# Kernel optimization log

Hardware: AMD Instinct MI355X
Metric: run time of the kernel (lower is better)

The kernel has to match this reference:

```python
import jax, jax.numpy as jnp
import numpy as np

N = 2048          # target nodes
N_NODES = 2048    # neighbor pool
D_IN = 256
D_EDGE = 16
D_HID = 32
D_OUT = 256


def _mlp(h, w1, b1, w2, b2):
    # Linear -> Tanh -> Linear
    return jnp.tanh(h @ w1 + b1) @ w2 + b2


def setup_inputs() -> dict:
    key = jax.random.key(0)
    ks = jax.random.split(key, 20)
    s = 0.05
    inp = {
        "x": jax.random.normal(ks[0], (N, D_IN), jnp.float32),
        "neibs": jax.random.normal(ks[1], (N_NODES, D_IN), jnp.float32),
        "edge_emb": jax.random.normal(ks[2], (N * N_NODES, D_EDGE), jnp.float32),
        # multiplicative binary mask (float, as in original ws * mask)
        "mask": (jax.random.uniform(ks[3], (N, N_NODES)) < 0.7).astype(jnp.float32),
        "ax_w1": jax.random.normal(ks[4], (D_IN, D_HID), jnp.float32) * s,
        "ax_b1": jnp.zeros((D_HID,), jnp.float32),
        "ax_w2": jax.random.normal(ks[5], (D_HID, D_HID), jnp.float32) * s,
        "ax_b2": jnp.zeros((D_HID,), jnp.float32),
        "an_w1": jax.random.normal(ks[6], (D_IN, D_HID), jnp.float32) * s,
        "an_b1": jnp.zeros((D_HID,), jnp.float32),
        "an_w2": jax.random.normal(ks[7], (D_HID, D_HID), jnp.float32) * s,
        "an_b2": jnp.zeros((D_HID,), jnp.float32),
        "ae_w1": jax.random.normal(ks[8], (D_EDGE, D_HID), jnp.float32) * s,
        "ae_b1": jnp.zeros((D_HID,), jnp.float32),
        "ae_w2": jax.random.normal(ks[9], (D_HID, D_HID), jnp.float32) * s,
        "ae_b2": jnp.zeros((D_HID,), jnp.float32),
        "fcx_w": jax.random.normal(ks[10], (2 * D_IN, D_OUT), jnp.float32) * s,
        "fcx_b": jnp.zeros((D_OUT,), jnp.float32),
    }
    return inp


def reference(x, neibs, edge_emb, mask,
              ax_w1, ax_b1, ax_w2, ax_b2,
              an_w1, an_b1, an_w2, an_b2,
              ae_w1, ae_b1, ae_w2, ae_b2,
              fcx_w, fcx_b):
    x_att = _mlp(x, ax_w1, ax_b1, ax_w2, ax_b2)          # (N, H)
    neib_att = _mlp(neibs, an_w1, an_b1, an_w2, an_b2)   # (n_nodes, H)
    # edge attention is computed in the original forward but never used (dead code)
    _edge_att = _mlp(edge_emb, ae_w1, ae_b1, ae_w2, ae_b2)
    # multiplicative masking (NOT additive -inf), then softmax over neighbors
    ws = jnp.einsum('nh,mh->nm', x_att, neib_att) * mask  # (N, n_nodes)
    ws = jax.nn.softmax(ws, axis=1)
    agg_neib = jax.nn.sigmoid(ws @ neibs)                 # (N, D_IN)
    # concat_node=False path: concat -> fc_x -> sigmoid; dropout is identity (eval)
    out = jax.nn.sigmoid(jnp.concatenate([x, agg_neib], axis=1) @ fcx_w + fcx_b)
    return out
```

## Files before the change

kernel.cpp:

```cpp
#include <hip/hip_runtime.h>
#include <hip/hip_bf16.h>
#include <math.h>

#define NROWS 2048
#define DIN 256
#define DH 32
#define DOUT 256

typedef unsigned short ushort_t;
typedef unsigned int uint_t;
typedef __attribute__((ext_vector_type(8))) short short8;
typedef __attribute__((ext_vector_type(4))) float floatx4;

__device__ __forceinline__ float bf2f(uint_t u) {
    union { uint_t i; float f; } v; v.i = u << 16; return v.f;
}
__device__ __forceinline__ ushort_t f2bf(float f) {
    __hip_bfloat16 h = __float2bfloat16(f);
    union { __hip_bfloat16 h; ushort_t u; } v; v.h = h; return v.u;
}
__device__ __forceinline__ float sigm(float v) { return 1.0f / (1.0f + __expf(-v)); }

#define PSTR 2056
#define ASTR 520

__global__ __launch_bounds__(256) void prep_kernel(
    const float* __restrict__ x, const float* __restrict__ neibs,
    const float* __restrict__ ax_w1, const float* __restrict__ ax_b1,
    const float* __restrict__ ax_w2, const float* __restrict__ ax_b2,
    const float* __restrict__ an_w1, const float* __restrict__ an_b1,
    const float* __restrict__ an_w2, const float* __restrict__ an_b2,
    const float* __restrict__ fcx_w,
    ushort_t* __restrict__ x_attB, short8* __restrict__ n_attP,
    short8* __restrict__ B_pack, short8* __restrict__ W_pack)
{
    __shared__ float smem[32 * 256];
    const int t = threadIdx.x;
    const int b = blockIdx.x;

    if (b < 512) {
        float (*srow)[DIN] = (float (*)[DIN])smem;
        float* hbuf = smem + 8 * DIN;
        float* sbuf = smem + 8 * DIN + 8 * DH;

        const bool is_x = b < 256;
        const int row0 = (is_x ? b : b - 256) * 8;
        const float* __restrict__ in = is_x ? x : neibs;
        const float* __restrict__ w1 = is_x ? ax_w1 : an_w1;
        const float* __restrict__ b1 = is_x ? ax_b1 : an_b1;
        const float* __restrict__ w2 = is_x ? ax_w2 : an_w2;
        const float* __restrict__ b2 = is_x ? ax_b2 : an_b2;

        const int r = t >> 5, c = t & 31;
        {
            const float4* in4 = (const float4*)(in + (size_t)(row0 + r) * DIN);
            float4 a = in4[c * 2], bb = in4[c * 2 + 1];
            *(float4*)&srow[r][c * 8] = a;
            *(float4*)&srow[r][c * 8 + 4] = bb;
        }
        __syncthreads();

        float s = b1[c];
#pragma unroll 8
        for (int k = 0; k < DIN; ++k) s += srow[r][k] * w1[k * DH + c];
        s = tanhf(s);
        hbuf[r * DH + c] = s;
        __syncthreads();

        float s2 = b2[c];
#pragma unroll
        for (int j = 0; j < DH; ++j) s2 += hbuf[r * DH + j] * w2[j * DH + c];

        if (is_x) {
            x_attB[(size_t)(row0 + r) * DH + c] = f2bf(s2);
        } else {
            sbuf[r * DH + c] = s2;
            __syncthreads();
            if (t < 32) {
                const int r2 = t >> 2, q = t & 3;
                const int row = row0 + r2;
                short8 v;
#pragma unroll
                for (int j = 0; j < 8; ++j) v[j] = (short)f2bf(sbuf[r2 * DH + q * 8 + j]);
                n_attP[(row >> 4) * 64 + q * 16 + (row & 15)] = v;
            }
        }
    } else if (b < 576) {
        const int s = b - 512;
        float* tile = smem;
#pragma unroll
        for (int i = 0; i < 8; ++i) {
            const int e = i * 256 + t;
            const int row = e >> 6, c4 = e & 63;
            const float4 v = ((const float4*)neibs)[(size_t)(32 * s + row) * 64 + c4];
            *(float4*)&tile[row * 256 + c4 * 4] = v;
        }
        __syncthreads();
#pragma unroll
        for (int i = 0; i < 4; ++i) {
            const int G = i * 256 + t;
            const int n = G & 15, q = (G >> 4) & 3, tt = (G >> 6) & 3, w = G >> 8;
            const int col = w * 64 + tt * 16 + n;
            short8 v;
#pragma unroll
            for (int j = 0; j < 8; ++j) v[j] = (short)f2bf(tile[(8 * q + j) * 256 + col]);
            B_pack[s * 1024 + G] = v;
        }
    } else {
        const int s = b - 576;
        float* tile = smem;
#pragma unroll
        for (int i = 0; i < 8; ++i) {
            const int e = i * 256 + t;
            const int row = e >> 6, c4 = e & 63;
            const float4 v = ((const float4*)fcx_w)[(size_t)(32 * s + row) * 64 + c4];
            *(float4*)&tile[row * 256 + c4 * 4] = v;
        }
        __syncthreads();
#pragma unroll
        for (int i = 0; i < 4; ++i) {
            const int G = i * 256 + t;
            const int n = G & 15, q = (G >> 4) & 3, tt = (G >> 6) & 3, w = G >> 8;
            const int col = w * 64 + tt * 16 + n;
            short8 v;
#pragma unroll
            for (int j = 0; j < 8; ++j) v[j] = (short)f2bf(tile[(8 * q + j) * 256 + col]);
            W_pack[s * 1024 + G] = v;
        }
    }
}

__global__ __launch_bounds__(512, 2) void attn_kernel(
    const float* __restrict__ x, const float* __restrict__ mask,
    const ushort_t* __restrict__ x_attB, const short8* __restrict__ n_attP,
    const short8* __restrict__ B_pack, const short8* __restrict__ W_pack,
    const float* __restrict__ fcx_b, float* __restrict__ out)
{
    __shared__ __align__(16) ushort_t pTr[8 * PSTR];
    __shared__ __align__(16) ushort_t ATr[8 * ASTR];
    __shared__ float row_inv[8];

    const int t = threadIdx.x;
    const int n0 = blockIdx.x * 8;
    const int w = t >> 6, lane = t & 63;
    const int q = lane >> 4, nn = lane & 15;
    const int arow = lane & 7;
    const int rbase = (lane >> 4) * 4;

#pragma unroll
    for (int i = 0; i < 4; ++i) {
        const int e = i * 512 + t;
        const int r = e >> 8, k = e & 255;
        ATr[r * ASTR + k] = f2bf(x[(size_t)(n0 + r) * DIN + k]);
    }

    const short8 av_s = *(const short8*)(x_attB + (size_t)(n0 + arow) * DH + q * 8);
#pragma unroll 4
    for (int i = 0; i < 16; ++i) {
        const int tl = w * 16 + i;
        const short8 bv = n_attP[tl * 64 + lane];
        floatx4 c = __builtin_amdgcn_mfma_f32_16x16x32_bf16(
            av_s, bv, (floatx4){0.f, 0.f, 0.f, 0.f}, 0, 0, 0);
        if (lane < 32) {
            const int m = tl * 16 + nn;
#pragma unroll
            for (int rg = 0; rg < 4; ++rg) {
                const int row = rbase + rg;
                const float sv = c[rg] * mask[(size_t)(n0 + row) * NROWS + m];
                pTr[row * PSTR + m] = f2bf(sv);
            }
        }
    }
    __syncthreads();

    {
        ushort_t* prow = pTr + w * PSTR;
        uint_t raw[16];
        float mx = -1e30f;
#pragma unroll
        for (int j = 0; j < 16; ++j) {
            raw[j] = *(const uint_t*)(prow + j * 128 + 2 * lane);
            mx = fmaxf(mx, fmaxf(bf2f(raw[j] & 0xffffu), bf2f(raw[j] >> 16)));
        }
#pragma unroll
        for (int off = 32; off >= 1; off >>= 1) mx = fmaxf(mx, __shfl_xor(mx, off));
        float sum = 0.f;
#pragma unroll
        for (int j = 0; j < 16; ++j) {
            const float e0 = __expf(bf2f(raw[j] & 0xffffu) - mx);
            const float e1 = __expf(bf2f(raw[j] >> 16) - mx);
            sum += e0 + e1;
            *(uint_t*)(prow + j * 128 + 2 * lane) =
                (uint_t)f2bf(e0) | ((uint_t)f2bf(e1) << 16);
        }
#pragma unroll
        for (int off = 32; off >= 1; off >>= 1) sum += __shfl_xor(sum, off);
        if (lane == 0) row_inv[w] = 1.f / sum;
    }
    __syncthreads();

    const int cq = w & 3, kh = w >> 2;
    const char* aBase = (const char*)pTr + arow * (PSTR * 2);
    floatx4 acc[4];
#pragma unroll
    for (int tt = 0; tt < 4; ++tt) acc[tt] = (floatx4){0.f, 0.f, 0.f, 0.f};

#pragma unroll 4
    for (int si = 0; si < 32; ++si) {
        const int s = kh * 32 + si;
        const short8 av = *(const short8*)(aBase + s * 64 + q * 16);
#pragma unroll
        for (int tt = 0; tt < 4; ++tt) {
            const short8 bv = B_pack[(s * 16 + cq * 4 + tt) * 64 + lane];
            acc[tt] = __builtin_amdgcn_mfma_f32_16x16x32_bf16(av, bv, acc[tt], 0, 0, 0);
        }
    }
    __syncthreads();
    float* red = (float*)pTr;
    if (kh == 1) {
#pragma unroll
        for (int tt = 0; tt < 4; ++tt)
            *(floatx4*)&red[((cq * 4 + tt) * 64 + lane) * 4] = acc[tt];
    }
    __syncthreads();
    if (kh == 0) {
#pragma unroll
        for (int tt = 0; tt < 4; ++tt) {
            const floatx4 rv = *(const floatx4*)&red[((cq * 4 + tt) * 64 + lane) * 4];
            acc[tt] += rv;
        }
        if (lane < 32) {
#pragma unroll
            for (int tt = 0; tt < 4; ++tt) {
                const int n = cq * 64 + tt * 16 + nn;
#pragma unroll
                for (int rg = 0; rg < 4; ++rg) {
                    const int row = rbase + rg;
                    ATr[row * ASTR + 256 + n] = f2bf(sigm(acc[tt][rg] * row_inv[row]));
                }
            }
        }
    }
    __syncthreads();

    const char* a2 = (const char*)ATr + arow * (ASTR * 2);
    floatx4 acc2[4];
#pragma unroll
    for (int tt = 0; tt < 4; ++tt) acc2[tt] = (floatx4){0.f, 0.f, 0.f, 0.f};

#pragma unroll
    for (int si = 0; si < 8; ++si) {
        const int s = kh * 8 + si;
        const short8 av = *(const short8*)(a2 + s * 64 + q * 16);
#pragma unroll
        for (int tt = 0; tt < 4; ++tt) {
            const short8 bv = W_pack[(s * 16 + cq * 4 + tt) * 64 + lane];
            acc2[tt] = __builtin_amdgcn_mfma_f32_16x16x32_bf16(av, bv, acc2[tt], 0, 0, 0);
        }
    }
    __syncthreads();
    if (kh == 1) {
#pragma unroll
        for (int tt = 0; tt < 4; ++tt)
            *(floatx4*)&red[((cq * 4 + tt) * 64 + lane) * 4] = acc2[tt];
    }
    __syncthreads();
    if (kh == 0) {
#pragma unroll
        for (int tt = 0; tt < 4; ++tt) {
            const floatx4 rv = *(const floatx4*)&red[((cq * 4 + tt) * 64 + lane) * 4];
            acc2[tt] += rv;
        }
        if (lane < 32) {
#pragma unroll
            for (int tt = 0; tt < 4; ++tt) {
                const int n = cq * 64 + tt * 16 + nn;
                const float bias = fcx_b[n];
#pragma unroll
                for (int rg = 0; rg < 4; ++rg) {
                    const int row = rbase + rg;
                    out[(size_t)(n0 + row) * DOUT + n] = sigm(acc2[tt][rg] + bias);
                }
            }
        }
    }
}

extern "C" void kernel_launch(void* const* d_in, const int* in_sizes, int n_in,
                              void* d_out, int out_size, void* d_ws, size_t ws_size,
                              hipStream_t stream) {
    const float* x      = (const float*)d_in[0];
    const float* neibs  = (const float*)d_in[1];
    const float* mask   = (const float*)d_in[3];
    const float* ax_w1  = (const float*)d_in[4];
    const float* ax_b1  = (const float*)d_in[5];
    const float* ax_w2  = (const float*)d_in[6];
    const float* ax_b2  = (const float*)d_in[7];
    const float* an_w1  = (const float*)d_in[8];
    const float* an_b1  = (const float*)d_in[9];
    const float* an_w2  = (const float*)d_in[10];
    const float* an_b2  = (const float*)d_in[11];
    const float* fcx_w  = (const float*)d_in[16];
    const float* fcx_b  = (const float*)d_in[17];
    float* out = (float*)d_out;

    char* ws = (char*)d_ws;
    ushort_t* x_attB = (ushort_t*)ws;
    short8*   n_attP = (short8*)(ws + 131072);
    short8*   B_pack = (short8*)(ws + 262144);
    short8*   W_pack = (short8*)(ws + 1310720);

    prep_kernel<<<592, 256, 0, stream>>>(
        x, neibs, ax_w1, ax_b1, ax_w2, ax_b2,
        an_w1, an_b1, an_w2, an_b2, fcx_w,
        x_attB, n_attP, B_pack, W_pack);

    attn_kernel<<<256, 512, 0, stream>>>(
        x, mask, x_attB, n_attP, B_pack, W_pack, fcx_b, out);
}
```

Baseline: 384.1 us.

## Split fused attention kernel into score, PV and FC GEMM kernels

Replaces the single fused attention kernel with three kernels. The first computes masked scores and the softmax, then writes normalized probabilities to a packed global buffer. The second does the P·neibs GEMM on 32-row by 64-column tiles, and the third does the final FC GEMM; x is converted to bf16 into a shared concat buffer during prep. The aim is to stop each 8-row block from streaming the whole packed neighbor matrix, which cuts L2/HBM traffic for B and raises MFMA reuse. In exchange it adds two kernel launches and a global round-trip for the probability and concat intermediates.

```diff
diff --git a/kernel.cpp b/kernel.cpp
--- a/kernel.cpp
+++ b/kernel.cpp
@@ -21,8 +21,7 @@
 }
 __device__ __forceinline__ float sigm(float v) { return 1.0f / (1.0f + __expf(-v)); }
 
-#define PSTR 2056
-#define ASTR 520
+#define PST 2056
 
 __global__ __launch_bounds__(256) void prep_kernel(
     const float* __restrict__ x, const float* __restrict__ neibs,
@@ -32,7 +31,8 @@
     const float* __restrict__ an_w2, const float* __restrict__ an_b2,
     const float* __restrict__ fcx_w,
     ushort_t* __restrict__ x_attB, short8* __restrict__ n_attP,
-    short8* __restrict__ B_pack, short8* __restrict__ W_pack)
+    short8* __restrict__ B_pack, short8* __restrict__ W_pack,
+    ushort_t* __restrict__ XA)
 {
     __shared__ float smem[32 * 256];
     const int t = threadIdx.x;
@@ -99,14 +99,14 @@
 #pragma unroll
         for (int i = 0; i < 4; ++i) {
             const int G = i * 256 + t;
-            const int n = G & 15, q = (G >> 4) & 3, tt = (G >> 6) & 3, w = G >> 8;
-            const int col = w * 64 + tt * 16 + n;
+            const int n = G & 15, q = (G >> 4) & 3, tl = G >> 6;
+            const int col = tl * 16 + n;
             short8 v;
 #pragma unroll
             for (int j = 0; j < 8; ++j) v[j] = (short)f2bf(tile[(8 * q + j) * 256 + col]);
-            B_pack[s * 1024 + G] = v;
-        }
-    } else {
+            B_pack[(size_t)(s * 16 + tl) * 64 + q * 16 + n] = v;
+        }
+    } else if (b < 592) {
         const int s = b - 576;
         float* tile = smem;
 #pragma unroll
@@ -120,169 +120,176 @@
 #pragma unroll
         for (int i = 0; i < 4; ++i) {
             const int G = i * 256 + t;
-            const int n = G & 15, q = (G >> 4) & 3, tt = (G >> 6) & 3, w = G >> 8;
-            const int col = w * 64 + tt * 16 + n;
+            const int n = G & 15, q = (G >> 4) & 3, tl = G >> 6;
+            const int col = tl * 16 + n;
             short8 v;
 #pragma unroll
             for (int j = 0; j < 8; ++j) v[j] = (short)f2bf(tile[(8 * q + j) * 256 + col]);
-            W_pack[s * 1024 + G] = v;
-        }
-    }
-}
-
-__global__ __launch_bounds__(512, 2) void attn_kernel(
-    const float* __restrict__ x, const float* __restrict__ mask,
+            W_pack[(size_t)(s * 16 + tl) * 64 + q * 16 + n] = v;
+        }
+    } else {
+        const int base = (b - 592) * 32;
+#pragma unroll
+        for (int j = 0; j < 32; ++j) {
+            const int row = base + j;
+            XA[(size_t)row * 512 + t] = f2bf(x[(size_t)row * DIN + t]);
+        }
+    }
+}
+
+__global__ __launch_bounds__(256) void score_kernel(
+    const float* __restrict__ mask,
     const ushort_t* __restrict__ x_attB, const short8* __restrict__ n_attP,
-    const short8* __restrict__ B_pack, const short8* __restrict__ W_pack,
+    short8* __restrict__ P_pack)
+{
+    __shared__ __align__(16) ushort_t pT[8 * PST];
+    __shared__ float row_inv[8];
+
+    const int t = threadIdx.x, b = blockIdx.x;
+    const int n0 = b * 8;
+    const int w = t >> 6, lane = t & 63;
+    const int q = lane >> 4, nn = lane & 15;
+
+    const short8 av = *(const short8*)(x_attB + (size_t)(n0 + (lane & 7)) * DH + q * 8);
+
+#pragma unroll 4
+    for (int i = 0; i < 32; ++i) {
+        const int tl = w * 32 + i;
+        const short8 bv = n_attP[tl * 64 + lane];
+        floatx4 c = __builtin_amdgcn_mfma_f32_16x16x32_bf16(
+            av, bv, (floatx4){0.f, 0.f, 0.f, 0.f}, 0, 0, 0);
+        if (lane < 32) {
+            const int m = tl * 16 + nn;
+            const int rbase = (lane >> 4) * 4;
+#pragma unroll
+            for (int rg = 0; rg < 4; ++rg) {
+                const int r = rbase + rg;
+                const float sv = c[rg] * mask[(size_t)(n0 + r) * NROWS + m];
+                pT[r * PST + m] = f2bf(sv);
+            }
+        }
+    }
+    __syncthreads();
+
+    {
+        const int r0 = 2 * w, r1 = r0 + 1;
+        ushort_t* p0 = pT + r0 * PST;
+        ushort_t* p1 = pT + r1 * PST;
+        float mx0 = -1e30f, mx1 = -1e30f;
+        uint_t raw0[16], raw1[16];
+#pragma unroll
+        for (int j = 0; j < 16; ++j) {
+            raw0[j] = *(const uint_t*)(p0 + j * 128 + 2 * lane);
+            raw1[j] = *(const uint_t*)(p1 + j * 128 + 2 * lane);
+            mx0 = fmaxf(mx0, fmaxf(bf2f(raw0[j] & 0xffffu), bf2f(raw0[j] >> 16)));
+            mx1 = fmaxf(mx1, fmaxf(bf2f(raw1[j] & 0xffffu), bf2f(raw1[j] >> 16)));
+        }
+#pragma unroll
+        for (int off = 32; off >= 1; off >>= 1) {
+            mx0 = fmaxf(mx0, __shfl_xor(mx0, off));
+            mx1 = fmaxf(mx1, __shfl_xor(mx1, off));
+        }
+        float l0 = 0.f, l1 = 0.f;
+#pragma unroll
+        for (int j = 0; j < 16; ++j) {
+            const float e00 = __expf(bf2f(raw0[j] & 0xffffu) - mx0);
+            const float e01 = __expf(bf2f(raw0[j] >> 16) - mx0);
+            const float e10 = __expf(bf2f(raw1[j] & 0xffffu) - mx1);
+            const float e11 = __expf(bf2f(raw1[j] >> 16) - mx1);
+            l0 += e00 + e01; l1 += e10 + e11;
+            *(uint_t*)(p0 + j * 128 + 2 * lane) = (uint_t)f2bf(e00) | ((uint_t)f2bf(e01) << 16);
+            *(uint_t*)(p1 + j * 128 + 2 * lane) = (uint_t)f2bf(e10) | ((uint_t)f2bf(e11) << 16);
+        }
+#pragma unroll
+        for (int off = 32; off >= 1; off >>= 1) {
+            l0 += __shfl_xor(l0, off);
+            l1 += __shfl_xor(l1, off);
+        }
+        if (lane == 0) { row_inv[r0] = 1.f / l0; row_inv[r1] = 1.f / l1; }
+    }
+    __syncthreads();
+
+    const int rt16 = b >> 1, h = b & 1;
+    const int sr = nn;
+    if ((sr >> 3) == h) {
+        const float invr = row_inv[sr & 7];
+        const ushort_t* prow = pT + (sr & 7) * PST;
+#pragma unroll
+        for (int i = 0; i < 16; ++i) {
+            const int s = w * 16 + i;
+            const short8 e = *(const short8*)(prow + 32 * s + 8 * q);
+            short8 v;
+#pragma unroll
+            for (int j = 0; j < 8; ++j)
+                v[j] = (short)f2bf(bf2f((uint_t)(ushort_t)e[j]) * invr);
+            P_pack[(size_t)(rt16 * 64 + s) * 64 + lane] = v;
+        }
+    }
+}
+
+__global__ __launch_bounds__(256) void pv_kernel(
+    const short8* __restrict__ P_pack, const short8* __restrict__ B_pack,
+    ushort_t* __restrict__ XA)
+{
+    const int t = threadIdx.x, b = blockIdx.x;
+    const int rt32 = b >> 2, cs = b & 3;
+    const int w = t >> 6, lane = t & 63;
+    const int ct = cs * 4 + w;
+
+    const short8* PA0 = P_pack + (size_t)(2 * rt32) * 64 * 64;
+    const short8* PA1 = PA0 + 64 * 64;
+
+    floatx4 a0 = (floatx4){0.f, 0.f, 0.f, 0.f};
+    floatx4 a1 = (floatx4){0.f, 0.f, 0.f, 0.f};
+#pragma unroll 4
+    for (int s = 0; s < 64; ++s) {
+        const short8 A0 = PA0[s * 64 + lane];
+        const short8 A1 = PA1[s * 64 + lane];
+        const short8 B  = B_pack[(size_t)(s * 16 + ct) * 64 + lane];
+        a0 = __builtin_amdgcn_mfma_f32_16x16x32_bf16(A0, B, a0, 0, 0, 0);
+        a1 = __builtin_amdgcn_mfma_f32_16x16x32_bf16(A1, B, a1, 0, 0, 0);
+    }
+
+    const int col = 16 * ct + (lane & 15);
+    const int rb = (lane >> 4) * 4;
+#pragma unroll
+    for (int rg = 0; rg < 4; ++rg) {
+        XA[(size_t)(32 * rt32 + rb + rg) * 512 + 256 + col] = f2bf(sigm(a0[rg]));
+        XA[(size_t)(32 * rt32 + 16 + rb + rg) * 512 + 256 + col] = f2bf(sigm(a1[rg]));
+    }
+}
+
+__global__ __launch_bounds__(256) void fc_kernel(
+    const ushort_t* __restrict__ XA, const short8* __restrict__ W_pack,
     const float* __restrict__ fcx_b, float* __restrict__ out)
 {
-    __shared__ __align__(16) ushort_t pTr[8 * PSTR];
-    __shared__ __align__(16) ushort_t ATr[8 * ASTR];
-    __shared__ float row_inv[8];
-
-    const int t = threadIdx.x;
-    const int n0 = blockIdx.x * 8;
+    const int t = threadIdx.x, b = blockIdx.x;
+    const int rt32 = b >> 2, cs = b & 3;
     const int w = t >> 6, lane = t & 63;
+    const int ct = cs * 4 + w;
     const int q = lane >> 4, nn = lane & 15;
-    const int arow = lane & 7;
-    const int rbase = (lane >> 4) * 4;
-
-#pragma unroll
-    for (int i = 0; i < 4; ++i) {
-        const int e = i * 512 + t;
-        const int r = e >> 8, k = e & 255;
-        ATr[r * ASTR + k] = f2bf(x[(size_t)(n0 + r) * DIN + k]);
-    }
-
-    const short8 av_s = *(const short8*)(x_attB + (size_t)(n0 + arow) * DH + q * 8);
-#pragma unroll 4
-    for (int i = 0; i < 16; ++i) {
-        const int tl = w * 16 + i;
-        const short8 bv = n_attP[tl * 64 + lane];
-        floatx4 c = __builtin_amdgcn_mfma_f32_16x16x32_bf16(
-            av_s, bv, (floatx4){0.f, 0.f, 0.f, 0.f}, 0, 0, 0);
-        if (lane < 32) {
-            const int m = tl * 16 + nn;
-#pragma unroll
-            for (int rg = 0; rg < 4; ++rg) {
-                const int row = rbase + rg;
-                const float sv = c[rg] * mask[(size_t)(n0 + row) * NROWS + m];
-                pTr[row * PSTR + m] = f2bf(sv);
-            }
-        }
-    }
-    __syncthreads();
-
-    {
-        ushort_t* prow = pTr + w * PSTR;
-        uint_t raw[16];
-        float mx = -1e30f;
-#pragma unroll
-        for (int j = 0; j < 16; ++j) {
-            raw[j] = *(const uint_t*)(prow + j * 128 + 2 * lane);
-            mx = fmaxf(mx, fmaxf(bf2f(raw[j] & 0xffffu), bf2f(raw[j] >> 16)));
-        }
-#pragma unroll
-        for (int off = 32; off >= 1; off >>= 1) mx = fmaxf(mx, __shfl_xor(mx, off));
-        float sum = 0.f;
-#pragma unroll
-        for (int j = 0; j < 16; ++j) {
-            const float e0 = __expf(bf2f(raw[j] & 0xffffu) - mx);
-            const float e1 = __expf(bf2f(raw[j] >> 16) - mx);
-            sum += e0 + e1;
-            *(uint_t*)(prow + j * 128 + 2 * lane) =
-                (uint_t)f2bf(e0) | ((uint_t)f2bf(e1) << 16);
-        }
-#pragma unroll
-        for (int off = 32; off >= 1; off >>= 1) sum += __shfl_xor(sum, off);
-        if (lane == 0) row_inv[w] = 1.f / sum;
-    }
-    __syncthreads();
-
-    const int cq = w & 3, kh = w >> 2;
-    const char* aBase = (const char*)pTr + arow * (PSTR * 2);
-    floatx4 acc[4];
-#pragma unroll
-    for (int tt = 0; tt < 4; ++tt) acc[tt] = (floatx4){0.f, 0.f, 0.f, 0.f};
-
-#pragma unroll 4
-    for (int si = 0; si < 32; ++si) {
-        const int s = kh * 32 + si;
-        const short8 av = *(const short8*)(aBase + s * 64 + q * 16);
-#pragma unroll
-        for (int tt = 0; tt < 4; ++tt) {
-            const short8 bv = B_pack[(s * 16 + cq * 4 + tt) * 64 + lane];
-            acc[tt] = __builtin_amdgcn_mfma_f32_16x16x32_bf16(av, bv, acc[tt], 0, 0, 0);
-        }
-    }
-    __syncthreads();
-    float* red = (float*)pTr;
-    if (kh == 1) {
-#pragma unroll
-        for (int tt = 0; tt < 4; ++tt)
-            *(floatx4*)&red[((cq * 4 + tt) * 64 + lane) * 4] = acc[tt];
-    }
-    __syncthreads();
-    if (kh == 0) {
-#pragma unroll
-        for (int tt = 0; tt < 4; ++tt) {
-            const floatx4 rv = *(const floatx4*)&red[((cq * 4 + tt) * 64 + lane) * 4];
-            acc[tt] += rv;
-        }
-        if (lane < 32) {
-#pragma unroll
-            for (int tt = 0; tt < 4; ++tt) {
-                const int n = cq * 64 + tt * 16 + nn;
-#pragma unroll
-                for (int rg = 0; rg < 4; ++rg) {
-                    const int row = rbase + rg;
-                    ATr[row * ASTR + 256 + n] = f2bf(sigm(acc[tt][rg] * row_inv[row]));
-                }
-            }
-        }
-    }
-    __syncthreads();
-
-    const char* a2 = (const char*)ATr + arow * (ASTR * 2);
-    floatx4 acc2[4];
-#pragma unroll
-    for (int tt = 0; tt < 4; ++tt) acc2[tt] = (floatx4){0.f, 0.f, 0.f, 0.f};
-
-#pragma unroll
-    for (int si = 0; si < 8; ++si) {
-        const int s = kh * 8 + si;
-        const short8 av = *(const short8*)(a2 + s * 64 + q * 16);
-#pragma unroll
-        for (int tt = 0; tt < 4; ++tt) {
-            const short8 bv = W_pack[(s * 16 + cq * 4 + tt) * 64 + lane];
-            acc2[tt] = __builtin_amdgcn_mfma_f32_16x16x32_bf16(av, bv, acc2[tt], 0, 0, 0);
-        }
-    }
-    __syncthreads();
-    if (kh == 1) {
-#pragma unroll
-        for (int tt = 0; tt < 4; ++tt)
-            *(floatx4*)&red[((cq * 4 + tt) * 64 + lane) * 4] = acc2[tt];
-    }
-    __syncthreads();
-    if (kh == 0) {
-#pragma unroll
-        for (int tt = 0; tt < 4; ++tt) {
-            const floatx4 rv = *(const floatx4*)&red[((cq * 4 + tt) * 64 + lane) * 4];
-            acc2[tt] += rv;
-        }
-        if (lane < 32) {
-#pragma unroll
-            for (int tt = 0; tt < 4; ++tt) {
-                const int n = cq * 64 + tt * 16 + nn;
-                const float bias = fcx_b[n];
-#pragma unroll
-                for (int rg = 0; rg < 4; ++rg) {
-                    const int row = rbase + rg;
-                    out[(size_t)(n0 + row) * DOUT + n] = sigm(acc2[tt][rg] + bias);
-                }
-            }
-        }
+
+    const ushort_t* X0 = XA + (size_t)(32 * rt32 + nn) * 512 + 8 * q;
+    const ushort_t* X1 = X0 + 16 * 512;
+
+    floatx4 a0 = (floatx4){0.f, 0.f, 0.f, 0.f};
+    floatx4 a1 = (floatx4){0.f, 0.f, 0.f, 0.f};
+#pragma unroll
+    for (int s = 0; s < 16; ++s) {
+        const short8 A0 = *(const short8*)(X0 + 32 * s);
+        const short8 A1 = *(const short8*)(X1 + 32 * s);
+        const short8 B  = W_pack[(size_t)(s * 16 + ct) * 64 + lane];
+        a0 = __builtin_amdgcn_mfma_f32_16x16x32_bf16(A0, B, a0, 0, 0, 0);
+        a1 = __builtin_amdgcn_mfma_f32_16x16x32_bf16(A1, B, a1, 0, 0, 0);
+    }
+
+    const int col = 16 * ct + nn;
+    const float bias = fcx_b[col];
+    const int rb = (lane >> 4) * 4;
+#pragma unroll
+    for (int rg = 0; rg < 4; ++rg) {
+        out[(size_t)(32 * rt32 + rb + rg) * DOUT + col] = sigm(a0[rg] + bias);
+        out[(size_t)(32 * rt32 + 16 + rb + rg) * DOUT + col] = sigm(a1[rg] + bias);
     }
 }
 
@@ -305,16 +312,21 @@
     float* out = (float*)d_out;
 
     char* ws = (char*)d_ws;
-    ushort_t* x_attB = (ushort_t*)ws;
+    ushort_t* x_attB = (ushort_t*)(ws);
     short8*   n_attP = (short8*)(ws + 131072);
     short8*   B_pack = (short8*)(ws + 262144);
     short8*   W_pack = (short8*)(ws + 1310720);
-
-    prep_kernel<<<592, 256, 0, stream>>>(
+    ushort_t* XA     = (ushort_t*)(ws + 1572864);
+    short8*   P_pack = (short8*)(ws + 3670016);
+
+    prep_kernel<<<656, 256, 0, stream>>>(
         x, neibs, ax_w1, ax_b1, ax_w2, ax_b2,
         an_w1, an_b1, an_w2, an_b2, fcx_w,
-        x_attB, n_attP, B_pack, W_pack);
-
-    attn_kernel<<<256, 512, 0, stream>>>(
-        x, mask, x_attB, n_attP, B_pack, W_pack, fcx_b, out);
-}
+        x_attB, n_attP, B_pack, W_pack, XA);
+
+    score_kernel<<<256, 256, 0, stream>>>(mask, x_attB, n_attP, P_pack);
+
+    pv_kernel<<<256, 256, 0, stream>>>(P_pack, B_pack, XA);
+
+    fc_kernel<<<256, 256, 0, stream>>>(XA, W_pack, fcx_b, out);
+}
```

After: 396.0 us. +3.1%, slower.
